# Kernel tuning notes

Measured on AMD Instinct MI355X. Metric: run time of the kernel, lower is better.

Reference implementation:

```python
import jax, jax.numpy as jnp
import numpy as np
import math

B, S, H, W = 1, 1024, 8, 32

def setup_inputs() -> dict:
    key = jax.random.key(0)
    kq, kk = jax.random.split(key)
    q = jax.random.normal(kq, (B, S, H, W), dtype=jnp.float32)
    k = jax.random.normal(kk, (B, S, H, W), dtype=jnp.float32)
    return {"q": q, "k": k}

def reference(q, k):
    # q: [b, s, h, w]; k: [b, t, h, w]
    # attn[b,s,t,h] = -sum_w |q[b,s,h,w] - k[b,t,h,w]| / sqrt(w)
    w = q.shape[-1]
    scale = 1.0 / math.sqrt(w)
    diff = jnp.abs(q[:, :, None, :, :] - k[:, None, :, :, :])  # [b,s,t,h,w]
    attn = -jnp.sum(diff, axis=-1) * scale                      # [b,s,t,h]
    return attn
```

## Files before the change

kernel.cpp:

```cpp
#include <hip/hip_runtime.h>


constexpr int S_DIM = 1024;
constexpr int T_DIM = 1024;
constexpr int H_DIM = 8;
constexpr int W_DIM = 32;
constexpr int TT = 64;
constexpr int SB = 16;
constexpr int MS = 4;

__global__ __launch_bounds__(256, 2)
void l1attn_kernel(const float* __restrict__ q,
                   const float* __restrict__ k,
                   float* __restrict__ out) {
    const int tid  = threadIdx.x;
    const int lane = tid & 63;
    const int wv   = tid >> 6;
    const int t0   = blockIdx.x * TT;
    const int s0   = blockIdx.y * SB + wv * MS;
    const int h    = lane & 7;
    const int tl   = lane >> 3;

    __shared__ float4 klds[TT * H_DIM * (W_DIM / 4)];

    float qreg[MS][W_DIM];
    #pragma unroll
    for (int si = 0; si < MS; ++si) {
        const float4* qrow =
            (const float4*)(q + ((size_t)(s0 + si) * H_DIM + h) * W_DIM);
        #pragma unroll
        for (int j = 0; j < 8; ++j) {
            float4 v = qrow[j];
            qreg[si][4 * j + 0] = v.x;
            qreg[si][4 * j + 1] = v.y;
            qreg[si][4 * j + 2] = v.z;
            qreg[si][4 * j + 3] = v.w;
        }
    }

    const float4* k4 = (const float4*)(k + (size_t)t0 * H_DIM * W_DIM);
    #pragma unroll
    for (int p = 0; p < 16; ++p) {
        int f = p * 256 + tid;
        int r = f >> 3;
        int j = f & 7;
        klds[r * 8 + (j ^ (r & 7))] = k4[f];
    }
    __syncthreads();

    const float nscale = -0.17677669529663688f;

    for (int tg = 0; tg < 8; ++tg) {
        const int r = tg * 64 + lane;
        const float4* krow = klds + r * 8;
        float kreg[W_DIM];
        #pragma unroll
        for (int j = 0; j < 8; ++j) {
            float4 v = krow[j ^ h];
            kreg[4 * j + 0] = v.x;
            kreg[4 * j + 1] = v.y;
            kreg[4 * j + 2] = v.z;
            kreg[4 * j + 3] = v.w;
        }
        const int t = t0 + tg * 8 + tl;
        #pragma unroll
        for (int si = 0; si < MS; ++si) {
            float a = 0.0f;
            #pragma unroll
            for (int w = 0; w < W_DIM; ++w)
                a += fabsf(qreg[si][w] - kreg[w]);
            out[((size_t)(s0 + si) * T_DIM + t) * H_DIM + h] = a * nscale;
        }
    }
}

extern "C" void kernel_launch(void* const* d_in, const int* in_sizes, int n_in,
                              void* d_out, int out_size, void* d_ws, size_t ws_size,
                              hipStream_t stream) {
    const float* q = (const float*)d_in[0];
    const float* k = (const float*)d_in[1];
    float* out = (float*)d_out;
    dim3 grid(T_DIM / TT, S_DIM / SB);
    l1attn_kernel<<<grid, dim3(256, 1, 1), 0, stream>>>(q, k, out);
}
```

Measured before the change: 87.50 us.

## Keep K row in registers and stream Q rows from global, dropping LDS

Restructures the kernel so each thread holds one K row (t,h) in registers and loops over 32 query rows, loading each Q row directly from global memory (which in practice is served by cache), instead of staging a K tile in shared memory and holding four Q rows per thread. This removes the LDS staging, the barrier and the register pressure from the qreg array, and raises the launch bound to 4 blocks per CU. It also splits the reduction into four partial accumulators to shorten the add dependency chain. The cost is repeated global/L1 loads of Q per thread, since every thread in a block reloads the same Q rows.

```diff
diff --git a/kernel.cpp b/kernel.cpp
--- a/kernel.cpp
+++ b/kernel.cpp
@@ -5,72 +5,51 @@
 constexpr int T_DIM = 1024;
 constexpr int H_DIM = 8;
 constexpr int W_DIM = 32;
-constexpr int TT = 64;
-constexpr int SB = 16;
-constexpr int MS = 4;
+constexpr int TB = 32;
+constexpr int SB = 32;
 
-__global__ __launch_bounds__(256, 2)
+__global__ __launch_bounds__(256, 4)
 void l1attn_kernel(const float* __restrict__ q,
                    const float* __restrict__ k,
                    float* __restrict__ out) {
     const int tid  = threadIdx.x;
-    const int lane = tid & 63;
-    const int wv   = tid >> 6;
-    const int t0   = blockIdx.x * TT;
-    const int s0   = blockIdx.y * SB + wv * MS;
-    const int h    = lane & 7;
-    const int tl   = lane >> 3;
+    const int h    = tid & 7;
+    const int tsub = tid >> 3;
+    const int t    = blockIdx.x * TB + tsub;
+    const int s0   = blockIdx.y * SB;
 
-    __shared__ float4 klds[TT * H_DIM * (W_DIM / 4)];
-
-    float qreg[MS][W_DIM];
-    #pragma unroll
-    for (int si = 0; si < MS; ++si) {
-        const float4* qrow =
-            (const float4*)(q + ((size_t)(s0 + si) * H_DIM + h) * W_DIM);
+    float kreg[W_DIM];
+    {
+        const float4* krow = (const float4*)(k + (t * H_DIM + h) * W_DIM);
         #pragma unroll
         for (int j = 0; j < 8; ++j) {
-            float4 v = qrow[j];
-            qreg[si][4 * j + 0] = v.x;
-            qreg[si][4 * j + 1] = v.y;
-            qreg[si][4 * j + 2] = v.z;
-            qreg[si][4 * j + 3] = v.w;
-        }
-    }
-
-    const float4* k4 = (const float4*)(k + (size_t)t0 * H_DIM * W_DIM);
-    #pragma unroll
-    for (int p = 0; p < 16; ++p) {
-        int f = p * 256 + tid;
-        int r = f >> 3;
-        int j = f & 7;
-        klds[r * 8 + (j ^ (r & 7))] = k4[f];
-    }
-    __syncthreads();
-
-    const float nscale = -0.17677669529663688f;
-
-    for (int tg = 0; tg < 8; ++tg) {
-        const int r = tg * 64 + lane;
-        const float4* krow = klds + r * 8;
-        float kreg[W_DIM];
-        #pragma unroll
-        for (int j = 0; j < 8; ++j) {
-            float4 v = krow[j ^ h];
+            float4 v = krow[j];
             kreg[4 * j + 0] = v.x;
             kreg[4 * j + 1] = v.y;
             kreg[4 * j + 2] = v.z;
             kreg[4 * j + 3] = v.w;
         }
-        const int t = t0 + tg * 8 + tl;
+    }
+
+    const float nscale = -0.17677669529663688f;
+
+    #pragma unroll 2
+    for (int si = 0; si < SB; ++si) {
+        const int s = s0 + si;
+        const float4* qrow = (const float4*)(q + (s * H_DIM + h) * W_DIM);
+        float4 qv[8];
         #pragma unroll
-        for (int si = 0; si < MS; ++si) {
-            float a = 0.0f;
-            #pragma unroll
-            for (int w = 0; w < W_DIM; ++w)
-                a += fabsf(qreg[si][w] - kreg[w]);
-            out[((size_t)(s0 + si) * T_DIM + t) * H_DIM + h] = a * nscale;
+        for (int j = 0; j < 8; ++j) qv[j] = qrow[j];
+
+        float a0 = 0.f, a1 = 0.f, a2 = 0.f, a3 = 0.f;
+        #pragma unroll
+        for (int j = 0; j < 8; ++j) {
+            a0 += fabsf(qv[j].x - kreg[4 * j + 0]);
+            a1 += fabsf(qv[j].y - kreg[4 * j + 1]);
+            a2 += fabsf(qv[j].z - kreg[4 * j + 2]);
+            a3 += fabsf(qv[j].w - kreg[4 * j + 3]);
         }
+        out[(s * T_DIM + t) * H_DIM + h] = ((a0 + a1) + (a2 + a3)) * nscale;
     }
 }
 
@@ -80,6 +59,6 @@
     const float* q = (const float*)d_in[0];
     const float* k = (const float*)d_in[1];
     float* out = (float*)d_out;
-    dim3 grid(T_DIM / TT, S_DIM / SB);
+    dim3 grid(T_DIM / TB, S_DIM / SB);
     l1attn_kernel<<<grid, dim3(256, 1, 1), 0, stream>>>(q, k, out);
 }
```

Result: slower. 213.9 us (+144.5%).
